# Performance work log

Measured on AMD Instinct MI355X. Metric: run time of the kernel, lower is better.

The kernel has to match this reference:

```python
import jax, jax.numpy as jnp
import numpy as np

B, T, H, DQK, DV = 2, 8192, 8, 128, 128
HID = H * DQK  # 1024
CHUNK = 64
EPS = 1e-5


def hedgehog(x, w, b):
    # torch Linear: y = x @ W.T + b, then softmax over cat([2y, -2y])
    y = x @ w.T + b
    return jax.nn.softmax(jnp.concatenate([2.0 * y, -2.0 * y], axis=-1), axis=-1)


def rmsnorm(x):
    return x * jax.lax.rsqrt(jnp.mean(x * x, axis=-1, keepdims=True) + EPS)


def chunk_linear_attn(q, k, v):
    # q, k: [B, T, H, Dk]; v: [B, T, H, Dv]  (head_first=False)
    scale = q.shape[-1] ** -0.5
    q = q * scale
    Bq, Tq, Hq, Dk = q.shape
    Dv = v.shape[-1]
    nc = Tq // CHUNK

    def to_chunks(t):
        # [B, T, H, D] -> [nc, B, H, C, D]
        return t.reshape(Bq, nc, CHUNK, Hq, -1).transpose(1, 0, 3, 2, 4)

    qc, kc, vc = to_chunks(q), to_chunks(k), to_chunks(v)
    mask = jnp.tril(jnp.ones((CHUNK, CHUNK), dtype=bool))

    def step(S, qkv):
        qi, ki, vi = qkv  # [B, H, C, D]
        attn = jnp.einsum('bhcd,bhed->bhce', qi, ki)      # intra-chunk scores
        attn = jnp.where(mask, attn, 0.0)                 # causal within chunk
        o = jnp.einsum('bhce,bhev->bhcv', attn, vi) \
            + jnp.einsum('bhcd,bhdv->bhcv', qi, S)        # inter-chunk via state
        S = S + jnp.einsum('bhcd,bhcv->bhdv', ki, vi)
        return S, o

    S0 = jnp.zeros((Bq, Hq, Dk, Dv), q.dtype)
    _, oc = jax.lax.scan(step, S0, (qc, kc, vc))          # oc: [nc, B, H, C, Dv]
    return oc.transpose(1, 0, 3, 2, 4).reshape(Bq, Tq, Hq, Dv)


def setup_inputs() -> dict:
    key = jax.random.key(0)
    ks = jax.random.split(key, 9)
    gain = 2.0 ** (-2.5)

    def xavier(k, shape):
        bound = gain * np.sqrt(6.0 / (shape[0] + shape[1]))
        return jax.random.uniform(k, shape, jnp.float32, -bound, bound)

    return {
        'x': jax.random.normal(ks[0], (B, T, HID), jnp.float32),
        'Wq': xavier(ks[1], (HID, HID)),
        'Wk': xavier(ks[2], (HID, HID)),
        'Wv': xavier(ks[3], (HID, HID)),
        'Wo': xavier(ks[4], (HID, HID)),
        # self.apply xavier-inits the hedgehog Linear layers too (no _is_hf_initialized flag)
        'fmq_w': xavier(ks[5], (DQK, DQK)),
        'fmq_b': jnp.zeros((DQK,), jnp.float32),
        'fmk_w': xavier(ks[6], (DQK, DQK)),
        'fmk_b': jnp.zeros((DQK,), jnp.float32),
    }


def reference(x, Wq, Wk, Wv, Wo, fmq_w, fmq_b, fmk_w, fmk_b):
    q = (x @ Wq.T).reshape(B, T, H, DQK)
    k = (x @ Wk.T).reshape(B, T, H, DQK)
    v = (x @ Wv.T).reshape(B, T, H, DV)
    q = hedgehog(q, fmq_w, fmq_b)   # [B, T, H, 2*DQK]
    k = hedgehog(k, fmk_w, fmk_b)   # [B, T, H, 2*DQK]
    o = chunk_linear_attn(q, k, v)  # [B, T, H, DV]
    o = rmsnorm(o.reshape(B, T, H * DV))
    return o @ Wo.T
```

## Files before the change

### kernel.cpp

```cpp
#include <hip/hip_runtime.h>
#include <stdint.h>

typedef unsigned short u16;
typedef __bf16 bf16x8 __attribute__((ext_vector_type(8)));
typedef float f32x4 __attribute__((ext_vector_type(4)));
typedef float f32x16 __attribute__((ext_vector_type(16)));

__device__ __forceinline__ u16 f2b(float f) {
  union { float f; unsigned u; } v; v.f = f;
  unsigned r = v.u + 0x7fffu + ((v.u >> 16) & 1u);
  return (u16)(r >> 16);
}
__device__ __forceinline__ float b2f(u16 b) {
  union { unsigned u; float f; } v; v.u = ((unsigned)b) << 16;
  return v.f;
}

__device__ __forceinline__ int swz64(int b) {
  return b ^ (((((b >> 6) & 3) ^ ((b >> 8) & 1))) << 4);
}

#define SB0() __builtin_amdgcn_sched_barrier(0)

__global__ __launch_bounds__(256) void cast_bf16(const float* __restrict__ in,
                                                 u16* __restrict__ out, int n4) {
  int i = blockIdx.x * 256 + threadIdx.x;
  if (i >= n4) return;
  float4 f = ((const float4*)in)[i];
  ushort4 r = make_ushort4(f2b(f.x), f2b(f.y), f2b(f.z), f2b(f.w));
  ((ushort4*)out)[i] = r;
}

__global__ __launch_bounds__(256) void fold_w(const float* __restrict__ W,
                                              const float* __restrict__ fmw,
                                              u16* __restrict__ out) {
  int hj = blockIdx.x;
  int h = hj >> 7, j = hj & 127;
  int i0 = threadIdx.x * 4;
  float a0 = 0.f, a1 = 0.f, a2 = 0.f, a3 = 0.f;
  const float* Wh = W + (size_t)(h * 128) * 1024 + i0;
  const float* fw = fmw + j * 128;
  for (int d = 0; d < 128; ++d) {
    float wv = fw[d];
    const float* wr = Wh + (size_t)d * 1024;
    a0 += wv * wr[0]; a1 += wv * wr[1]; a2 += wv * wr[2]; a3 += wv * wr[3];
  }
  ushort4 r = make_ushort4(f2b(a0), f2b(a1), f2b(a2), f2b(a3));
  ((ushort4*)(out + (size_t)hj * 1024))[threadIdx.x] = r;
}

__global__ __launch_bounds__(512, 2) void gemm256(const u16* __restrict__ A,
                                                  const u16* __restrict__ B,
                                                  u16* __restrict__ C,
                                                  int M, int N, int K, int LNT) {
  __shared__ u16 lds[65536];
  const int tid = threadIdx.x, w = tid >> 6, lane = tid & 63;
  int g = blockIdx.x;
  int wg = (g & 7) * ((int)gridDim.x >> 3) + (g >> 3);
  const int nt = wg & ((1 << LNT) - 1), mt = wg >> LNT;
  const int m0 = mt << 8, n0 = nt << 8;
  const int wm = w >> 2, wn = w & 3;
  const int fm = lane & 15, fkb = (lane >> 4) << 4;

  int so0 = w * 1024 + lane * 16;
  int so1 = so0 + 8192;
  const int p0s = swz64(so0), p1s = swz64(so1);
  const size_t ga0 = (size_t)(p0s >> 6) * K + ((p0s & 63) >> 1);
  const size_t ga1 = (size_t)(p1s >> 6) * K + ((p1s & 63) >> 1);
  so0 >>= 1; so1 >>= 1;
#define STAGE(g0, slot)                                                               \
  do {                                                                                \
    __builtin_amdgcn_global_load_lds(                                                 \
        (const __attribute__((address_space(1))) unsigned int*)((g0) + ga0),          \
        (__attribute__((address_space(3))) unsigned int*)((slot) + so0), 16, 0, 0);   \
    __builtin_amdgcn_global_load_lds(                                                 \
        (const __attribute__((address_space(1))) unsigned int*)((g0) + ga1),          \
        (__attribute__((address_space(3))) unsigned int*)((slot) + so1), 16, 0, 0);   \
  } while (0)

  int aoff[2][4], boff[4];
#pragma unroll
  for (int mh = 0; mh < 2; ++mh)
#pragma unroll
    for (int mi = 0; mi < 4; ++mi)
      aoff[mh][mi] = swz64((wm * 128 + mh * 64 + mi * 16 + fm) * 64 + fkb) >> 1;
#pragma unroll
  for (int ni = 0; ni < 4; ++ni)
    boff[ni] = swz64((wn * 64 + ni * 16 + fm) * 64 + fkb) >> 1;

  const u16* Ag = A + (size_t)m0 * K;
  const u16* Bg = B + (size_t)n0 * K;
  const int NT = K >> 6;
  f32x4 acc[8][4] = {};

  STAGE(Ag, lds);
  STAGE(Bg, lds + 32768);
  STAGE(Ag + 32, lds + 8192);
  STAGE(Bg + 32, lds + 32768 + 8192);
  STAGE(Ag + 64, lds + 16384);
  STAGE(Bg + 64, lds + 32768 + 16384);
  asm volatile("s_waitcnt vmcnt(4)" ::: "memory");
  __builtin_amdgcn_s_barrier();

  for (int t = 0; t < NT; ++t) {
    const int buf = t & 1, nb = buf ^ 1;
    const u16* As0 = lds + buf * 16384;
    const u16* As1 = As0 + 8192;
    const u16* Bs0 = lds + 32768 + buf * 16384;
    const u16* Bs1 = Bs0 + 8192;
    bf16x8 a[4], bfr[4];

#pragma unroll
    for (int mi = 0; mi < 4; ++mi) a[mi] = *(const bf16x8*)(As0 + aoff[0][mi]);
#pragma unroll
    for (int ni = 0; ni < 4; ++ni) bfr[ni] = *(const bf16x8*)(Bs0 + boff[ni]);
    if (t + 1 < NT) STAGE(Ag + (t + 1) * 64 + 32, lds + nb * 16384 + 8192);
    __builtin_amdgcn_s_barrier();
    asm volatile("s_waitcnt lgkmcnt(0)" ::: "memory");
    SB0();
    __builtin_amdgcn_s_setprio(1);
#pragma unroll
    for (int mi = 0; mi < 4; ++mi)
#pragma unroll
      for (int ni = 0; ni < 4; ++ni)
        acc[mi][ni] = __builtin_amdgcn_mfma_f32_16x16x32_bf16(a[mi], bfr[ni], acc[mi][ni], 0, 0, 0);
    __builtin_amdgcn_s_setprio(0);
    __builtin_amdgcn_s_barrier();

#pragma unroll
    for (int mi = 0; mi < 4; ++mi) a[mi] = *(const bf16x8*)(As0 + aoff[1][mi]);
    if (t + 1 < NT) STAGE(Bg + (t + 1) * 64 + 32, lds + 32768 + nb * 16384 + 8192);
    __builtin_amdgcn_s_barrier();
    asm volatile("s_waitcnt lgkmcnt(0)" ::: "memory");
    SB0();
    __builtin_amdgcn_s_setprio(1);
#pragma unroll
    for (int mi = 0; mi < 4; ++mi)
#pragma unroll
      for (int ni = 0; ni < 4; ++ni)
        acc[4 + mi][ni] =
            __builtin_amdgcn_mfma_f32_16x16x32_bf16(a[mi], bfr[ni], acc[4 + mi][ni], 0, 0, 0);
    __builtin_amdgcn_s_setprio(0);
    __builtin_amdgcn_s_barrier();

#pragma unroll
    for (int mi = 0; mi < 4; ++mi) a[mi] = *(const bf16x8*)(As1 + aoff[0][mi]);
#pragma unroll
    for (int ni = 0; ni < 4; ++ni) bfr[ni] = *(const bf16x8*)(Bs1 + boff[ni]);
    if (t + 2 < NT) STAGE(Ag + (t + 2) * 64, lds + buf * 16384);
    __builtin_amdgcn_s_barrier();
    asm volatile("s_waitcnt lgkmcnt(0)" ::: "memory");
    SB0();
    __builtin_amdgcn_s_setprio(1);
#pragma unroll
    for (int mi = 0; mi < 4; ++mi)
#pragma unroll
      for (int ni = 0; ni < 4; ++ni)
        acc[mi][ni] = __builtin_amdgcn_mfma_f32_16x16x32_bf16(a[mi], bfr[ni], acc[mi][ni], 0, 0, 0);
    __builtin_amdgcn_s_setprio(0);
    __builtin_amdgcn_s_barrier();

#pragma unroll
    for (int mi = 0; mi < 4; ++mi) a[mi] = *(const bf16x8*)(As1 + aoff[1][mi]);
    if (t + 2 < NT) STAGE(Bg + (t + 2) * 64, lds + 32768 + buf * 16384);
    __builtin_amdgcn_s_barrier();
    asm volatile("s_waitcnt lgkmcnt(0)" ::: "memory");
    SB0();
    __builtin_amdgcn_s_setprio(1);
#pragma unroll
    for (int mi = 0; mi < 4; ++mi)
#pragma unroll
      for (int ni = 0; ni < 4; ++ni)
        acc[4 + mi][ni] =
            __builtin_amdgcn_mfma_f32_16x16x32_bf16(a[mi], bfr[ni], acc[4 + mi][ni], 0, 0, 0);
    __builtin_amdgcn_s_setprio(0);
    if (t < NT - 2)
      asm volatile("s_waitcnt vmcnt(4)" ::: "memory");
    else
      asm volatile("s_waitcnt vmcnt(0)" ::: "memory");
    __builtin_amdgcn_s_barrier();
  }
#undef STAGE

  u16* Cs = lds;
  const int cr = (lane >> 4) << 2, cc = lane & 15;
#pragma unroll
  for (int am = 0; am < 8; ++am)
#pragma unroll
    for (int ni = 0; ni < 4; ++ni)
#pragma unroll
      for (int r = 0; r < 4; ++r)
        Cs[(wm * 128 + (am >> 2) * 64 + (am & 3) * 16 + cr + r) * 256 + wn * 64 + ni * 16 + cc] =
            f2b(acc[am][ni][r]);
  __syncthreads();
#pragma unroll
  for (int pass = 0; pass < 16; ++pass) {
    int row = pass * 16 + (tid >> 5);
    int colb = (tid & 31) << 4;
    *(uint4*)((char*)(C + (size_t)(m0 + row) * N + n0) + colb) =
        *(const uint4*)((const char*)(Cs + row * 256) + colb);
  }
}

template <int OUT_BF16>
__global__ __launch_bounds__(256) void gemm_bt(const u16* __restrict__ A,
                                               const u16* __restrict__ B,
                                               void* __restrict__ Cv,
                                               int M, int N, int K, int SWZ, int LNT) {
  __shared__ u16 smem[16384];
  u16* As = smem;
  u16* Bs = smem + 8192;
  const int tid = threadIdx.x;
  int g = blockIdx.y * gridDim.x + blockIdx.x;
  int xcd = g & 7, local = g >> 3;
  int mt, nt;
  if (SWZ == 0) {
    mt = xcd * ((int)gridDim.y >> 3) + (local >> LNT);
    nt = local & ((1 << LNT) - 1);
  } else {
    nt = xcd * ((int)gridDim.x >> 3) + (local >> 3);
    mt = local & 7;
  }
  const int m0 = mt * 128, n0 = nt * 128;
  const int wave = tid >> 6, lane = tid & 63;
  const int wm = (wave >> 1) << 6, wn = (wave & 1) << 6;
  f32x4 acc[4][4] = {};
  const int srow = tid >> 3;
  const int scol = (tid & 7) << 3;
  const u16* Ab = A + (size_t)(m0 + srow) * K + scol;
  const u16* Bb = B + (size_t)(n0 + srow) * K + scol;
  u16* Asp = As + srow * 64 + scol;
  u16* Bsp = Bs + srow * 64 + scol;
  const int fm = lane & 15;
  const int fk = (lane >> 4) << 3;
  for (int kt = 0; kt < K; kt += 64) {
#pragma unroll
    for (int i = 0; i < 4; ++i) {
      __builtin_amdgcn_global_load_lds(
          (__attribute__((address_space(1))) unsigned int*)(Ab + (size_t)i * 32 * K + kt),
          (__attribute__((address_space(3))) unsigned int*)(Asp + i * 32 * 64), 16, 0, 0);
      __builtin_amdgcn_global_load_lds(
          (__attribute__((address_space(1))) unsigned int*)(Bb + (size_t)i * 32 * K + kt),
          (__attribute__((address_space(3))) unsigned int*)(Bsp + i * 32 * 64), 16, 0, 0);
    }
    __syncthreads();
#pragma unroll
    for (int kb = 0; kb < 2; ++kb) {
      bf16x8 af[4], bfr[4];
#pragma unroll
      for (int i = 0; i < 4; ++i)
        af[i] = *(const bf16x8*)(As + (wm + i * 16 + fm) * 64 + kb * 32 + fk);
#pragma unroll
      for (int j = 0; j < 4; ++j)
        bfr[j] = *(const bf16x8*)(Bs + (wn + j * 16 + fm) * 64 + kb * 32 + fk);
#pragma unroll
      for (int i = 0; i < 4; ++i)
#pragma unroll
        for (int j = 0; j < 4; ++j)
          acc[i][j] = __builtin_amdgcn_mfma_f32_16x16x32_bf16(af[i], bfr[j], acc[i][j], 0, 0, 0);
    }
    __syncthreads();
  }
  const int cr = (lane >> 4) << 2;
  const int cc = lane & 15;
  if (OUT_BF16) {
    u16* Cs = smem;
#pragma unroll
    for (int i = 0; i < 4; ++i)
#pragma unroll
      for (int j = 0; j < 4; ++j)
#pragma unroll
        for (int r = 0; r < 4; ++r)
          Cs[(wm + i * 16 + cr + r) * 128 + wn + j * 16 + cc] = f2b(acc[i][j][r]);
    __syncthreads();
    u16* Cg = (u16*)Cv;
#pragma unroll
    for (int i = 0; i < 8; ++i) {
      int row = (i >> 1) * 32 + (tid >> 3);
      int col = ((i & 1) * 8 + (tid & 7)) * 8;
      *(uint4*)(Cg + (size_t)(m0 + row) * N + n0 + col) = *(const uint4*)(Cs + row * 128 + col);
    }
  } else {
    float* Csf = (float*)smem;
    float* Cg = (float*)Cv;
#pragma unroll
    for (int hh = 0; hh < 2; ++hh) {
      __syncthreads();
      if ((wm >> 6) == hh) {
#pragma unroll
        for (int i = 0; i < 4; ++i)
#pragma unroll
          for (int j = 0; j < 4; ++j)
#pragma unroll
            for (int r = 0; r < 4; ++r)
              Csf[(i * 16 + cr + r) * 128 + wn + j * 16 + cc] = acc[i][j][r];
      }
      __syncthreads();
#pragma unroll
      for (int i = 0; i < 8; ++i) {
        int row = (i >> 1) * 16 + (tid >> 4);
        int col = ((i & 1) * 16 + (tid & 15)) * 4;
        *(float4*)(Cg + (size_t)(m0 + hh * 64 + row) * N + n0 + col) =
            *(const float4*)(Csf + row * 128 + col);
      }
    }
  }
}

__global__ __launch_bounds__(256) void hedgehog_sm(const u16* __restrict__ y,
                                                   const float* __restrict__ bias,
                                                   u16* __restrict__ phi, float scale,
                                                   int colbase) {
  int wave = threadIdx.x >> 6, lane = threadIdx.x & 63;
  int rh = blockIdx.x * 4 + wave;
  const u16* yr = y + (size_t)(rh >> 3) * 2048 + colbase + (rh & 7) * 128;
  float a1 = 2.f * (b2f(yr[lane]) + bias[lane]);
  float a2 = 2.f * (b2f(yr[lane + 64]) + bias[lane + 64]);
  float mx = fmaxf(fabsf(a1), fabsf(a2));
#pragma unroll
  for (int off = 32; off; off >>= 1) mx = fmaxf(mx, __shfl_xor(mx, off, 64));
  float e1 = __expf(a1 - mx), e2 = __expf(a2 - mx);
  float n1 = __expf(-a1 - mx), n2 = __expf(-a2 - mx);
  float s = e1 + e2 + n1 + n2;
#pragma unroll
  for (int off = 32; off; off >>= 1) s += __shfl_xor(s, off, 64);
  float inv = scale / s;
  u16* pr = phi + (size_t)rh * 256;
  pr[lane] = f2b(e1 * inv);
  pr[lane + 64] = f2b(e2 * inv);
  pr[lane + 128] = f2b(n1 * inv);
  pr[lane + 192] = f2b(n2 * inv);
}

__global__ __launch_bounds__(256, 1) void attn_intra64(const u16* __restrict__ phi_q,
                                                       const u16* __restrict__ phi_k,
                                                       const u16* __restrict__ vt,
                                                       float* __restrict__ o,
                                                       u16* __restrict__ kv) {
  __shared__ u16 lds[18432];
  u16* At = lds;
  u16* Kt = lds;
  int g = blockIdx.x;
  int n = g & 127, h = g >> 7;
  int t0 = n * 64;
  const u16* qg = phi_q + ((size_t)t0 * 8 + h) * 256;
  const u16* kg = phi_k + ((size_t)t0 * 8 + h) * 256;
  const u16* vg = vt + (size_t)(h * 128) * 8192 + t0;
  int tid = threadIdx.x, lane = tid & 63, w = tid >> 6;
  const int fr = lane & 31, fg = (lane >> 5) << 3;
  const int rbase = (lane >> 5) << 2;
  const int mw = (w >> 1) << 5;
  const int nw = (w & 1) << 5;
  const int nv = (w & 1) << 6;

  f32x16 accS = {};
#pragma unroll
  for (int ks = 0; ks < 16; ++ks) {
    bf16x8 a = *(const bf16x8*)(qg + (size_t)(mw + fr) * 2048 + ks * 16 + fg);
    bf16x8 b = *(const bf16x8*)(kg + (size_t)(nw + fr) * 2048 + ks * 16 + fg);
    accS = __builtin_amdgcn_mfma_f32_32x32x16_bf16(a, b, accS, 0, 0, 0);
  }
  {
    int col = nw + (lane & 31);
#pragma unroll
    for (int r = 0; r < 16; ++r) {
      int row = mw + (r & 3) + ((r >> 2) << 3) + rbase;
      At[row * 136 + col] = f2b(col <= row ? accS[r] : 0.f);
    }
  }
  __syncthreads();
  f32x16 accO[2] = {};
#pragma unroll
  for (int ks = 0; ks < 4; ++ks) {
    bf16x8 a = *(const bf16x8*)(At + (mw + fr) * 136 + ks * 16 + fg);
#pragma unroll
    for (int nj = 0; nj < 2; ++nj) {
      bf16x8 b = *(const bf16x8*)(vg + (size_t)(nv + nj * 32 + fr) * 8192 + ks * 16 + fg);
      accO[nj] = __builtin_amdgcn_mfma_f32_32x32x16_bf16(a, b, accO[nj], 0, 0, 0);
    }
  }
  {
    float* og = o + ((size_t)t0 * 8 + h) * 128;
#pragma unroll
    for (int nj = 0; nj < 2; ++nj) {
      int vc = nv + nj * 32 + (lane & 31);
#pragma unroll
      for (int r = 0; r < 16; ++r) {
        int row = mw + (r & 3) + ((r >> 2) << 3) + rbase;
        og[(size_t)row * 1024 + vc] = accO[nj][r];
      }
    }
  }
  __syncthreads();

  {
    int r4 = (tid & 15) << 2;
    int d0 = (tid >> 4) << 4;
    u16 tmp[4][16];
#pragma unroll
    for (int r = 0; r < 4; ++r) {
      const u16* src = kg + (size_t)(r4 + r) * 2048 + d0;
      *(uint4*)(tmp[r]) = *(const uint4*)src;
      *(uint4*)(tmp[r] + 8) = *(const uint4*)(src + 8);
    }
#pragma unroll
    for (int jj = 0; jj < 16; ++jj) {
      ushort4 pk = make_ushort4(tmp[0][jj], tmp[1][jj], tmp[2][jj], tmp[3][jj]);
      *(ushort4*)(Kt + (d0 + jj) * 72 + r4) = pk;
    }
  }
  __syncthreads();
  const int nd = w << 6;
  f32x16 accKV[4][2] = {};
#pragma unroll
  for (int ks = 0; ks < 4; ++ks) {
    bf16x8 a[4], b[2];
#pragma unroll
    for (int mi = 0; mi < 4; ++mi)
      a[mi] = *(const bf16x8*)(vg + (size_t)(mi * 32 + fr) * 8192 + ks * 16 + fg);
#pragma unroll
    for (int nj = 0; nj < 2; ++nj)
      b[nj] = *(const bf16x8*)(Kt + (nd + nj * 32 + fr) * 72 + ks * 16 + fg);
#pragma unroll
    for (int mi = 0; mi < 4; ++mi)
#pragma unroll
      for (int nj = 0; nj < 2; ++nj)
        accKV[mi][nj] =
            __builtin_amdgcn_mfma_f32_32x32x16_bf16(a[mi], b[nj], accKV[mi][nj], 0, 0, 0);
  }
  {
    u16* kvg = kv + (size_t)g * 32768;
#pragma unroll
    for (int mi = 0; mi < 4; ++mi)
#pragma unroll
      for (int nj = 0; nj < 2; ++nj) {
        f32x16 acc = accKV[mi][nj];
        int d = nd + nj * 32 + (lane & 31);
#pragma unroll
        for (int r = 0; r < 16; ++r) {
          int vc = mi * 32 + (r & 3) + ((r >> 2) << 3) + rbase;
          kvg[(size_t)vc * 256 + d] = f2b(acc[r]);
        }
      }
  }
}

__global__ __launch_bounds__(256) void kv_scan64(u16* __restrict__ kv) {
  int idx = blockIdx.x * 256 + threadIdx.x;
  int h = idx >> 13;
  int e4 = idx & 8191;
  u16* p = kv + (size_t)h * 4194304 + (size_t)e4 * 4;
  float run[4] = {};
#pragma unroll 4
  for (int nn = 0; nn < 128; ++nn) {
    uint2 raw = *(const uint2*)p;
    u16* rv = (u16*)&raw;
    uint2 outw;
    u16* ov = (u16*)&outw;
#pragma unroll
    for (int i = 0; i < 4; ++i) {
      float v = b2f(rv[i]);
      ov[i] = f2b(run[i]);
      run[i] += v;
    }
    *(uint2*)p = outw;
    p += 32768;
  }
}

__global__ __launch_bounds__(256, 1) void attn_inter64(const u16* __restrict__ phi_q,
                                                       const u16* __restrict__ kv,
                                                       float* __restrict__ o) {
  int g = blockIdx.x;
  int n = g & 127, h = g >> 7;
  int t0 = n * 64;
  const u16* qg = phi_q + ((size_t)t0 * 8 + h) * 256;
  const u16* sg = kv + (size_t)g * 32768;
  int tid = threadIdx.x, lane = tid & 63, w = tid >> 6;
  const int fr = lane & 31, fg = (lane >> 5) << 3;
  const int rbase = (lane >> 5) << 2;
  const int mw = (w >> 1) << 5;
  const int nv = (w & 1) << 6;
  f32x16 acc[2] = {};
#pragma unroll
  for (int ks = 0; ks < 16; ++ks) {
    bf16x8 a = *(const bf16x8*)(qg + (size_t)(mw + fr) * 2048 + ks * 16 + fg);
#pragma unroll
    for (int nj = 0; nj < 2; ++nj) {
      bf16x8 b = *(const bf16x8*)(sg + (size_t)(nv + nj * 32 + fr) * 256 + ks * 16 + fg);
      acc[nj] = __builtin_amdgcn_mfma_f32_32x32x16_bf16(a, b, acc[nj], 0, 0, 0);
    }
  }
  float* og = o + ((size_t)t0 * 8 + h) * 128;
#pragma unroll
  for (int nj = 0; nj < 2; ++nj) {
    int vc = nv + nj * 32 + (lane & 31);
#pragma unroll
    for (int r = 0; r < 16; ++r) {
      int row = mw + (r & 3) + ((r >> 2) << 3) + rbase;
      og[(size_t)row * 1024 + vc] += acc[nj][r];
    }
  }
}

__global__ __launch_bounds__(256) void rmsnorm_k(const float* __restrict__ o,
                                                 u16* __restrict__ on) {
  __shared__ float red[4];
  int row = blockIdx.x;
  const float* orow = o + (size_t)row * 1024;
  int tid = threadIdx.x;
  float4 v = ((const float4*)orow)[tid];
  float ss = v.x * v.x + v.y * v.y + v.z * v.z + v.w * v.w;
#pragma unroll
  for (int off = 32; off; off >>= 1) ss += __shfl_xor(ss, off, 64);
  if ((tid & 63) == 0) red[tid >> 6] = ss;
  __syncthreads();
  float tot = red[0] + red[1] + red[2] + red[3];
  float rms = rsqrtf(tot * (1.f / 1024.f) + 1e-5f);
  ushort4 r = make_ushort4(f2b(v.x * rms), f2b(v.y * rms), f2b(v.z * rms), f2b(v.w * rms));
  ((ushort4*)(on + (size_t)row * 1024))[tid] = r;
}

extern "C" void kernel_launch(void* const* d_in, const int* in_sizes, int n_in,
                              void* d_out, int out_size, void* d_ws, size_t ws_size,
                              hipStream_t stream) {
  const float* x     = (const float*)d_in[0];
  const float* Wq    = (const float*)d_in[1];
  const float* Wk    = (const float*)d_in[2];
  const float* Wv    = (const float*)d_in[3];
  const float* Wo    = (const float*)d_in[4];
  const float* fmq_w = (const float*)d_in[5];
  const float* fmq_b = (const float*)d_in[6];
  const float* fmk_w = (const float*)d_in[7];
  const float* fmk_b = (const float*)d_in[8];

  char* ws = (char*)d_ws;
  u16*   kvb  = (u16*)(ws + 0);
  u16*   xb   = (u16*)(ws + 0);
  u16*   yb   = (u16*)(ws + 16777216);
  u16*   onb  = (u16*)(ws + 50331648);
  u16*   phiq = (u16*)(ws + 67108864);
  u16*   phik = (u16*)(ws + 100663296);
  u16*   vtb  = (u16*)(ws + 134217728);
  float* obuf = (float*)(ws + 150994944);
  u16*   wqkc = (u16*)(ws + 184549376);
  u16*   wvb  = (u16*)(ws + 188743680);
  u16*   wob  = (u16*)(ws + 190840832);

  cast_bf16<<<1024, 256, 0, stream>>>(Wv, wvb, 262144);
  cast_bf16<<<1024, 256, 0, stream>>>(Wo, wob, 262144);
  fold_w<<<1024, 256, 0, stream>>>(Wq, fmq_w, wqkc);
  fold_w<<<1024, 256, 0, stream>>>(Wk, fmk_w, wqkc + 1048576);

  for (int b = 0; b < 2; ++b) {
    const float* xsrc = x + (size_t)b * 8388608;
    float* osrc = (float*)d_out + (size_t)b * 8388608;
    cast_bf16<<<8192, 256, 0, stream>>>(xsrc, xb, 2097152);
    gemm256<<<256, 512, 0, stream>>>(xb, wqkc, yb, 8192, 2048, 1024, 3);
    hedgehog_sm<<<16384, 256, 0, stream>>>(yb, fmq_b, phiq, 0.0625f, 0);
    hedgehog_sm<<<16384, 256, 0, stream>>>(yb, fmk_b, phik, 1.0f, 1024);
    gemm_bt<1><<<dim3(64, 8), 256, 0, stream>>>(wvb, xb, vtb, 1024, 8192, 1024, 1, 0);
    attn_intra64<<<1024, 256, 0, stream>>>(phiq, phik, vtb, obuf, kvb);
    kv_scan64<<<256, 256, 0, stream>>>(kvb);
    attn_inter64<<<1024, 256, 0, stream>>>(phiq, kvb, obuf);
    rmsnorm_k<<<8192, 256, 0, stream>>>(obuf, onb);
    gemm_bt<0><<<dim3(8, 64), 256, 0, stream>>>(onb, wob, osrc, 8192, 1024, 1024, 0, 3);
  }
}
```

Measured before the change: 656.0 us.

## Reuse 256-tile GEMM for V and output projections; fuse intra and inter attention

The smaller 128-tile gemm_bt kernel is replaced by a templated gemm256 that can write fp32 output, and that kernel now handles both the V projection and the output projection. Attention is reorganised so one kernel computes only the per-chunk KV states. A fused kernel then computes the intra-chunk and inter-chunk outputs together and writes o once, instead of writing it and later doing a read-modify-write. The larger tiles give only 128 workgroups for 1024-wide N, so the GPU may be underfilled, and the intra scores are now computed after the scan.

```diff
diff --git a/kernel.cpp b/kernel.cpp
--- a/kernel.cpp
+++ b/kernel.cpp
@@ -49,9 +49,10 @@
   ((ushort4*)(out + (size_t)hj * 1024))[threadIdx.x] = r;
 }
 
+template <int OUT_BF16>
 __global__ __launch_bounds__(512, 2) void gemm256(const u16* __restrict__ A,
                                                   const u16* __restrict__ B,
-                                                  u16* __restrict__ C,
+                                                  void* __restrict__ Cv,
                                                   int M, int N, int K, int LNT) {
   __shared__ u16 lds[65536];
   const int tid = threadIdx.x, w = tid >> 6, lane = tid & 63;
@@ -182,126 +183,49 @@
   }
 #undef STAGE
 
-  u16* Cs = lds;
   const int cr = (lane >> 4) << 2, cc = lane & 15;
-#pragma unroll
-  for (int am = 0; am < 8; ++am)
-#pragma unroll
-    for (int ni = 0; ni < 4; ++ni)
-#pragma unroll
-      for (int r = 0; r < 4; ++r)
-        Cs[(wm * 128 + (am >> 2) * 64 + (am & 3) * 16 + cr + r) * 256 + wn * 64 + ni * 16 + cc] =
-            f2b(acc[am][ni][r]);
-  __syncthreads();
-#pragma unroll
-  for (int pass = 0; pass < 16; ++pass) {
-    int row = pass * 16 + (tid >> 5);
-    int colb = (tid & 31) << 4;
-    *(uint4*)((char*)(C + (size_t)(m0 + row) * N + n0) + colb) =
-        *(const uint4*)((const char*)(Cs + row * 256) + colb);
-  }
-}
-
-template <int OUT_BF16>
-__global__ __launch_bounds__(256) void gemm_bt(const u16* __restrict__ A,
-                                               const u16* __restrict__ B,
-                                               void* __restrict__ Cv,
-                                               int M, int N, int K, int SWZ, int LNT) {
-  __shared__ u16 smem[16384];
-  u16* As = smem;
-  u16* Bs = smem + 8192;
-  const int tid = threadIdx.x;
-  int g = blockIdx.y * gridDim.x + blockIdx.x;
-  int xcd = g & 7, local = g >> 3;
-  int mt, nt;
-  if (SWZ == 0) {
-    mt = xcd * ((int)gridDim.y >> 3) + (local >> LNT);
-    nt = local & ((1 << LNT) - 1);
+  if (OUT_BF16) {
+    u16* Cs = lds;
+    u16* Cg = (u16*)Cv;
+#pragma unroll
+    for (int am = 0; am < 8; ++am)
+#pragma unroll
+      for (int ni = 0; ni < 4; ++ni)
+#pragma unroll
+        for (int r = 0; r < 4; ++r)
+          Cs[(wm * 128 + (am >> 2) * 64 + (am & 3) * 16 + cr + r) * 256 + wn * 64 + ni * 16 + cc] =
+              f2b(acc[am][ni][r]);
+    __syncthreads();
+#pragma unroll
+    for (int pass = 0; pass < 16; ++pass) {
+      int row = pass * 16 + (tid >> 5);
+      int colb = (tid & 31) << 4;
+      *(uint4*)((char*)(Cg + (size_t)(m0 + row) * N + n0) + colb) =
+          *(const uint4*)((const char*)(Cs + row * 256) + colb);
+    }
   } else {
-    nt = xcd * ((int)gridDim.x >> 3) + (local >> 3);
-    mt = local & 7;
-  }
-  const int m0 = mt * 128, n0 = nt * 128;
-  const int wave = tid >> 6, lane = tid & 63;
-  const int wm = (wave >> 1) << 6, wn = (wave & 1) << 6;
-  f32x4 acc[4][4] = {};
-  const int srow = tid >> 3;
-  const int scol = (tid & 7) << 3;
-  const u16* Ab = A + (size_t)(m0 + srow) * K + scol;
-  const u16* Bb = B + (size_t)(n0 + srow) * K + scol;
-  u16* Asp = As + srow * 64 + scol;
-  u16* Bsp = Bs + srow * 64 + scol;
-  const int fm = lane & 15;
-  const int fk = (lane >> 4) << 3;
-  for (int kt = 0; kt < K; kt += 64) {
-#pragma unroll
-    for (int i = 0; i < 4; ++i) {
-      __builtin_amdgcn_global_load_lds(
-          (__attribute__((address_space(1))) unsigned int*)(Ab + (size_t)i * 32 * K + kt),
-          (__attribute__((address_space(3))) unsigned int*)(Asp + i * 32 * 64), 16, 0, 0);
-      __builtin_amdgcn_global_load_lds(
-          (__attribute__((address_space(1))) unsigned int*)(Bb + (size_t)i * 32 * K + kt),
-          (__attribute__((address_space(3))) unsigned int*)(Bsp + i * 32 * 64), 16, 0, 0);
-    }
-    __syncthreads();
-#pragma unroll
-    for (int kb = 0; kb < 2; ++kb) {
-      bf16x8 af[4], bfr[4];
-#pragma unroll
-      for (int i = 0; i < 4; ++i)
-        af[i] = *(const bf16x8*)(As + (wm + i * 16 + fm) * 64 + kb * 32 + fk);
-#pragma unroll
-      for (int j = 0; j < 4; ++j)
-        bfr[j] = *(const bf16x8*)(Bs + (wn + j * 16 + fm) * 64 + kb * 32 + fk);
-#pragma unroll
-      for (int i = 0; i < 4; ++i)
-#pragma unroll
-        for (int j = 0; j < 4; ++j)
-          acc[i][j] = __builtin_amdgcn_mfma_f32_16x16x32_bf16(af[i], bfr[j], acc[i][j], 0, 0, 0);
-    }
-    __syncthreads();
-  }
-  const int cr = (lane >> 4) << 2;
-  const int cc = lane & 15;
-  if (OUT_BF16) {
-    u16* Cs = smem;
-#pragma unroll
-    for (int i = 0; i < 4; ++i)
-#pragma unroll
-      for (int j = 0; j < 4; ++j)
-#pragma unroll
-        for (int r = 0; r < 4; ++r)
-          Cs[(wm + i * 16 + cr + r) * 128 + wn + j * 16 + cc] = f2b(acc[i][j][r]);
-    __syncthreads();
-    u16* Cg = (u16*)Cv;
-#pragma unroll
-    for (int i = 0; i < 8; ++i) {
-      int row = (i >> 1) * 32 + (tid >> 3);
-      int col = ((i & 1) * 8 + (tid & 7)) * 8;
-      *(uint4*)(Cg + (size_t)(m0 + row) * N + n0 + col) = *(const uint4*)(Cs + row * 128 + col);
-    }
-  } else {
-    float* Csf = (float*)smem;
+    float* Csf = (float*)lds;
     float* Cg = (float*)Cv;
 #pragma unroll
     for (int hh = 0; hh < 2; ++hh) {
       __syncthreads();
-      if ((wm >> 6) == hh) {
-#pragma unroll
-        for (int i = 0; i < 4; ++i)
-#pragma unroll
-          for (int j = 0; j < 4; ++j)
+      if (wm == hh) {
+#pragma unroll
+        for (int am = 0; am < 8; ++am)
+#pragma unroll
+          for (int ni = 0; ni < 4; ++ni)
 #pragma unroll
             for (int r = 0; r < 4; ++r)
-              Csf[(i * 16 + cr + r) * 128 + wn + j * 16 + cc] = acc[i][j][r];
+              Csf[((am >> 2) * 64 + (am & 3) * 16 + cr + r) * 256 + wn * 64 + ni * 16 + cc] =
+                  acc[am][ni][r];
       }
       __syncthreads();
 #pragma unroll
-      for (int i = 0; i < 8; ++i) {
-        int row = (i >> 1) * 16 + (tid >> 4);
-        int col = ((i & 1) * 16 + (tid & 15)) * 4;
-        *(float4*)(Cg + (size_t)(m0 + hh * 64 + row) * N + n0 + col) =
-            *(const float4*)(Csf + row * 128 + col);
+      for (int it = 0; it < 16; ++it) {
+        int row = it * 8 + (tid >> 6);
+        int colb = (tid & 63) << 2;
+        *(float4*)(Cg + (size_t)(m0 + hh * 128 + row) * N + n0 + colb) =
+            *(const float4*)(Csf + row * 256 + colb);
       }
     }
   }
@@ -332,66 +256,18 @@
   pr[lane + 192] = f2b(n2 * inv);
 }
 
-__global__ __launch_bounds__(256, 1) void attn_intra64(const u16* __restrict__ phi_q,
-                                                       const u16* __restrict__ phi_k,
-                                                       const u16* __restrict__ vt,
-                                                       float* __restrict__ o,
-                                                       u16* __restrict__ kv) {
-  __shared__ u16 lds[18432];
-  u16* At = lds;
-  u16* Kt = lds;
+__global__ __launch_bounds__(256, 1) void attn_kv64(const u16* __restrict__ phi_k,
+                                                    const u16* __restrict__ vt,
+                                                    u16* __restrict__ kv) {
+  __shared__ u16 Kt[18432];
   int g = blockIdx.x;
   int n = g & 127, h = g >> 7;
   int t0 = n * 64;
-  const u16* qg = phi_q + ((size_t)t0 * 8 + h) * 256;
   const u16* kg = phi_k + ((size_t)t0 * 8 + h) * 256;
   const u16* vg = vt + (size_t)(h * 128) * 8192 + t0;
   int tid = threadIdx.x, lane = tid & 63, w = tid >> 6;
   const int fr = lane & 31, fg = (lane >> 5) << 3;
   const int rbase = (lane >> 5) << 2;
-  const int mw = (w >> 1) << 5;
-  const int nw = (w & 1) << 5;
-  const int nv = (w & 1) << 6;
-
-  f32x16 accS = {};
-#pragma unroll
-  for (int ks = 0; ks < 16; ++ks) {
-    bf16x8 a = *(const bf16x8*)(qg + (size_t)(mw + fr) * 2048 + ks * 16 + fg);
-    bf16x8 b = *(const bf16x8*)(kg + (size_t)(nw + fr) * 2048 + ks * 16 + fg);
-    accS = __builtin_amdgcn_mfma_f32_32x32x16_bf16(a, b, accS, 0, 0, 0);
-  }
-  {
-    int col = nw + (lane & 31);
-#pragma unroll
-    for (int r = 0; r < 16; ++r) {
-      int row = mw + (r & 3) + ((r >> 2) << 3) + rbase;
-      At[row * 136 + col] = f2b(col <= row ? accS[r] : 0.f);
-    }
-  }
-  __syncthreads();
-  f32x16 accO[2] = {};
-#pragma unroll
-  for (int ks = 0; ks < 4; ++ks) {
-    bf16x8 a = *(const bf16x8*)(At + (mw + fr) * 136 + ks * 16 + fg);
-#pragma unroll
-    for (int nj = 0; nj < 2; ++nj) {
-      bf16x8 b = *(const bf16x8*)(vg + (size_t)(nv + nj * 32 + fr) * 8192 + ks * 16 + fg);
-      accO[nj] = __builtin_amdgcn_mfma_f32_32x32x16_bf16(a, b, accO[nj], 0, 0, 0);
-    }
-  }
-  {
-    float* og = o + ((size_t)t0 * 8 + h) * 128;
-#pragma unroll
-    for (int nj = 0; nj < 2; ++nj) {
-      int vc = nv + nj * 32 + (lane & 31);
-#pragma unroll
-      for (int r = 0; r < 16; ++r) {
-        int row = mw + (r & 3) + ((r >> 2) << 3) + rbase;
-        og[(size_t)row * 1024 + vc] = accO[nj][r];
-      }
-    }
-  }
-  __syncthreads();
 
   {
     int r4 = (tid & 15) << 2;
@@ -468,37 +344,71 @@
   }
 }
 
-__global__ __launch_bounds__(256, 1) void attn_inter64(const u16* __restrict__ phi_q,
+__global__ __launch_bounds__(256, 1) void attn_fused64(const u16* __restrict__ phi_q,
+                                                       const u16* __restrict__ phi_k,
+                                                       const u16* __restrict__ vt,
                                                        const u16* __restrict__ kv,
                                                        float* __restrict__ o) {
+  __shared__ u16 At[8704];
   int g = blockIdx.x;
   int n = g & 127, h = g >> 7;
   int t0 = n * 64;
   const u16* qg = phi_q + ((size_t)t0 * 8 + h) * 256;
+  const u16* kg = phi_k + ((size_t)t0 * 8 + h) * 256;
+  const u16* vg = vt + (size_t)(h * 128) * 8192 + t0;
   const u16* sg = kv + (size_t)g * 32768;
   int tid = threadIdx.x, lane = tid & 63, w = tid >> 6;
   const int fr = lane & 31, fg = (lane >> 5) << 3;
   const int rbase = (lane >> 5) << 2;
   const int mw = (w >> 1) << 5;
+  const int nw = (w & 1) << 5;
   const int nv = (w & 1) << 6;
-  f32x16 acc[2] = {};
+
+  f32x16 accS = {};
 #pragma unroll
   for (int ks = 0; ks < 16; ++ks) {
     bf16x8 a = *(const bf16x8*)(qg + (size_t)(mw + fr) * 2048 + ks * 16 + fg);
+    bf16x8 b = *(const bf16x8*)(kg + (size_t)(nw + fr) * 2048 + ks * 16 + fg);
+    accS = __builtin_amdgcn_mfma_f32_32x32x16_bf16(a, b, accS, 0, 0, 0);
+  }
+  {
+    int col = nw + (lane & 31);
+#pragma unroll
+    for (int r = 0; r < 16; ++r) {
+      int row = mw + (r & 3) + ((r >> 2) << 3) + rbase;
+      At[row * 136 + col] = f2b(col <= row ? accS[r] : 0.f);
+    }
+  }
+  __syncthreads();
+  f32x16 accO[2] = {};
+#pragma unroll
+  for (int ks = 0; ks < 4; ++ks) {
+    bf16x8 a = *(const bf16x8*)(At + (mw + fr) * 136 + ks * 16 + fg);
+#pragma unroll
+    for (int nj = 0; nj < 2; ++nj) {
+      bf16x8 b = *(const bf16x8*)(vg + (size_t)(nv + nj * 32 + fr) * 8192 + ks * 16 + fg);
+      accO[nj] = __builtin_amdgcn_mfma_f32_32x32x16_bf16(a, b, accO[nj], 0, 0, 0);
+    }
+  }
+#pragma unroll
+  for (int ks = 0; ks < 16; ++ks) {
+    bf16x8 a = *(const bf16x8*)(qg + (size_t)(mw + fr) * 2048 + ks * 16 + fg);
 #pragma unroll
     for (int nj = 0; nj < 2; ++nj) {
       bf16x8 b = *(const bf16x8*)(sg + (size_t)(nv + nj * 32 + fr) * 256 + ks * 16 + fg);
-      acc[nj] = __builtin_amdgcn_mfma_f32_32x32x16_bf16(a, b, acc[nj], 0, 0, 0);
-    }
-  }
-  float* og = o + ((size_t)t0 * 8 + h) * 128;
-#pragma unroll
-  for (int nj = 0; nj < 2; ++nj) {
-    int vc = nv + nj * 32 + (lane & 31);
-#pragma unroll
-    for (int r = 0; r < 16; ++r) {
-      int row = mw + (r & 3) + ((r >> 2) << 3) + rbase;
-      og[(size_t)row * 1024 + vc] += acc[nj][r];
+      accO[nj] = __builtin_amdgcn_mfma_f32_32x32x16_bf16(a, b, accO[nj], 0, 0, 0);
+    }
+  }
+  {
+    float* og = o + ((size_t)t0 * 8 + h) * 128;
+#pragma unroll
+    for (int nj = 0; nj < 2; ++nj) {
+      int vc = nv + nj * 32 + (lane & 31);
+#pragma unroll
+      for (int r = 0; r < 16; ++r) {
+        int row = mw + (r & 3) + ((r >> 2) << 3) + rbase;
+        og[(size_t)row * 1024 + vc] = accO[nj][r];
+      }
     }
   }
 }
@@ -556,14 +466,14 @@
     const float* xsrc = x + (size_t)b * 8388608;
     float* osrc = (float*)d_out + (size_t)b * 8388608;
     cast_bf16<<<8192, 256, 0, stream>>>(xsrc, xb, 2097152);
-    gemm256<<<256, 512, 0, stream>>>(xb, wqkc, yb, 8192, 2048, 1024, 3);
+    gemm256<1><<<256, 512, 0, stream>>>(xb, wqkc, yb, 8192, 2048, 1024, 3);
     hedgehog_sm<<<16384, 256, 0, stream>>>(yb, fmq_b, phiq, 0.0625f, 0);
     hedgehog_sm<<<16384, 256, 0, stream>>>(yb, fmk_b, phik, 1.0f, 1024);
-    gemm_bt<1><<<dim3(64, 8), 256, 0, stream>>>(wvb, xb, vtb, 1024, 8192, 1024, 1, 0);
-    attn_intra64<<<1024, 256, 0, stream>>>(phiq, phik, vtb, obuf, kvb);
+    gemm256<1><<<128, 512, 0, stream>>>(wvb, xb, vtb, 1024, 8192, 1024, 5);
+    attn_kv64<<<1024, 256, 0, stream>>>(phik, vtb, kvb);
     kv_scan64<<<256, 256, 0, stream>>>(kvb);
-    attn_inter64<<<1024, 256, 0, stream>>>(phiq, kvb, obuf);
+    attn_fused64<<<1024, 256, 0, stream>>>(phiq, phik, vtb, kvb, obuf);
     rmsnorm_k<<<8192, 256, 0, stream>>>(obuf, onb);
-    gemm_bt<0><<<dim3(8, 64), 256, 0, stream>>>(onb, wob, osrc, 8192, 1024, 1024, 0, 3);
-  }
-}
+    gemm256<0><<<128, 512, 0, stream>>>(onb, wob, osrc, 8192, 1024, 1024, 2);
+  }
+}
```

Result: slower. 702.5 us (+7.1%).

## Fuse intra-chunk attention with inter-chunk state product into one kernel

Applied to the files above, without the earlier changes.

Moves the intra-chunk QK^T and causal AV computation out of the KV-building kernel and into the inter-chunk kernel, which now computes Q·S and QK^T from Q fragments held in registers, then accumulates the masked AV into the same accumulators. This removes the fp32 write of the intra-chunk output followed by its read-modify-write in the inter kernel, and loads Q once instead of twice. The fused kernel uses more registers for the cached Q fragments, and the phi_k and V chunk reads now happen in both kernels.

```diff
diff --git a/kernel.cpp b/kernel.cpp
--- a/kernel.cpp
+++ b/kernel.cpp
@@ -332,66 +332,18 @@
   pr[lane + 192] = f2b(n2 * inv);
 }
 
-__global__ __launch_bounds__(256, 1) void attn_intra64(const u16* __restrict__ phi_q,
-                                                       const u16* __restrict__ phi_k,
-                                                       const u16* __restrict__ vt,
-                                                       float* __restrict__ o,
-                                                       u16* __restrict__ kv) {
-  __shared__ u16 lds[18432];
-  u16* At = lds;
-  u16* Kt = lds;
+__global__ __launch_bounds__(256, 1) void attn_kv64(const u16* __restrict__ phi_k,
+                                                    const u16* __restrict__ vt,
+                                                    u16* __restrict__ kv) {
+  __shared__ u16 Kt[18432];
   int g = blockIdx.x;
   int n = g & 127, h = g >> 7;
   int t0 = n * 64;
-  const u16* qg = phi_q + ((size_t)t0 * 8 + h) * 256;
   const u16* kg = phi_k + ((size_t)t0 * 8 + h) * 256;
   const u16* vg = vt + (size_t)(h * 128) * 8192 + t0;
   int tid = threadIdx.x, lane = tid & 63, w = tid >> 6;
   const int fr = lane & 31, fg = (lane >> 5) << 3;
   const int rbase = (lane >> 5) << 2;
-  const int mw = (w >> 1) << 5;
-  const int nw = (w & 1) << 5;
-  const int nv = (w & 1) << 6;
-
-  f32x16 accS = {};
-#pragma unroll
-  for (int ks = 0; ks < 16; ++ks) {
-    bf16x8 a = *(const bf16x8*)(qg + (size_t)(mw + fr) * 2048 + ks * 16 + fg);
-    bf16x8 b = *(const bf16x8*)(kg + (size_t)(nw + fr) * 2048 + ks * 16 + fg);
-    accS = __builtin_amdgcn_mfma_f32_32x32x16_bf16(a, b, accS, 0, 0, 0);
-  }
-  {
-    int col = nw + (lane & 31);
-#pragma unroll
-    for (int r = 0; r < 16; ++r) {
-      int row = mw + (r & 3) + ((r >> 2) << 3) + rbase;
-      At[row * 136 + col] = f2b(col <= row ? accS[r] : 0.f);
-    }
-  }
-  __syncthreads();
-  f32x16 accO[2] = {};
-#pragma unroll
-  for (int ks = 0; ks < 4; ++ks) {
-    bf16x8 a = *(const bf16x8*)(At + (mw + fr) * 136 + ks * 16 + fg);
-#pragma unroll
-    for (int nj = 0; nj < 2; ++nj) {
-      bf16x8 b = *(const bf16x8*)(vg + (size_t)(nv + nj * 32 + fr) * 8192 + ks * 16 + fg);
-      accO[nj] = __builtin_amdgcn_mfma_f32_32x32x16_bf16(a, b, accO[nj], 0, 0, 0);
-    }
-  }
-  {
-    float* og = o + ((size_t)t0 * 8 + h) * 128;
-#pragma unroll
-    for (int nj = 0; nj < 2; ++nj) {
-      int vc = nv + nj * 32 + (lane & 31);
-#pragma unroll
-      for (int r = 0; r < 16; ++r) {
-        int row = mw + (r & 3) + ((r >> 2) << 3) + rbase;
-        og[(size_t)row * 1024 + vc] = accO[nj][r];
-      }
-    }
-  }
-  __syncthreads();
 
   {
     int r4 = (tid & 15) << 2;
@@ -468,37 +420,77 @@
   }
 }
 
-__global__ __launch_bounds__(256, 1) void attn_inter64(const u16* __restrict__ phi_q,
+__global__ __launch_bounds__(256, 1) void attn_fused64(const u16* __restrict__ phi_q,
+                                                       const u16* __restrict__ phi_k,
+                                                       const u16* __restrict__ vt,
                                                        const u16* __restrict__ kv,
                                                        float* __restrict__ o) {
+  __shared__ u16 At[8704];
   int g = blockIdx.x;
   int n = g & 127, h = g >> 7;
   int t0 = n * 64;
   const u16* qg = phi_q + ((size_t)t0 * 8 + h) * 256;
+  const u16* kg = phi_k + ((size_t)t0 * 8 + h) * 256;
+  const u16* vg = vt + (size_t)(h * 128) * 8192 + t0;
   const u16* sg = kv + (size_t)g * 32768;
   int tid = threadIdx.x, lane = tid & 63, w = tid >> 6;
   const int fr = lane & 31, fg = (lane >> 5) << 3;
   const int rbase = (lane >> 5) << 2;
   const int mw = (w >> 1) << 5;
+  const int nw = (w & 1) << 5;
   const int nv = (w & 1) << 6;
-  f32x16 acc[2] = {};
-#pragma unroll
-  for (int ks = 0; ks < 16; ++ks) {
-    bf16x8 a = *(const bf16x8*)(qg + (size_t)(mw + fr) * 2048 + ks * 16 + fg);
-#pragma unroll
-    for (int nj = 0; nj < 2; ++nj) {
-      bf16x8 b = *(const bf16x8*)(sg + (size_t)(nv + nj * 32 + fr) * 256 + ks * 16 + fg);
-      acc[nj] = __builtin_amdgcn_mfma_f32_32x32x16_bf16(a, b, acc[nj], 0, 0, 0);
-    }
-  }
-  float* og = o + ((size_t)t0 * 8 + h) * 128;
-#pragma unroll
-  for (int nj = 0; nj < 2; ++nj) {
-    int vc = nv + nj * 32 + (lane & 31);
+
+  bf16x8 qf[16];
+  {
+    const u16* qrow = qg + (size_t)(mw + fr) * 2048 + fg;
+#pragma unroll
+    for (int ks = 0; ks < 16; ++ks) qf[ks] = *(const bf16x8*)(qrow + ks * 16);
+  }
+
+  f32x16 accS = {};
+  f32x16 accO[2] = {};
+  {
+    const u16* krow = kg + (size_t)(nw + fr) * 2048 + fg;
+    const u16* srow0 = sg + (size_t)(nv + fr) * 256 + fg;
+    const u16* srow1 = sg + (size_t)(nv + 32 + fr) * 256 + fg;
+#pragma unroll
+    for (int ks = 0; ks < 16; ++ks) {
+      bf16x8 kb = *(const bf16x8*)(krow + ks * 16);
+      bf16x8 sb0 = *(const bf16x8*)(srow0 + ks * 16);
+      bf16x8 sb1 = *(const bf16x8*)(srow1 + ks * 16);
+      accS = __builtin_amdgcn_mfma_f32_32x32x16_bf16(qf[ks], kb, accS, 0, 0, 0);
+      accO[0] = __builtin_amdgcn_mfma_f32_32x32x16_bf16(qf[ks], sb0, accO[0], 0, 0, 0);
+      accO[1] = __builtin_amdgcn_mfma_f32_32x32x16_bf16(qf[ks], sb1, accO[1], 0, 0, 0);
+    }
+  }
+  {
+    int col = nw + (lane & 31);
 #pragma unroll
     for (int r = 0; r < 16; ++r) {
       int row = mw + (r & 3) + ((r >> 2) << 3) + rbase;
-      og[(size_t)row * 1024 + vc] += acc[nj][r];
+      At[row * 136 + col] = f2b(col <= row ? accS[r] : 0.f);
+    }
+  }
+  __syncthreads();
+#pragma unroll
+  for (int ks = 0; ks < 4; ++ks) {
+    bf16x8 a = *(const bf16x8*)(At + (mw + fr) * 136 + ks * 16 + fg);
+#pragma unroll
+    for (int nj = 0; nj < 2; ++nj) {
+      bf16x8 b = *(const bf16x8*)(vg + (size_t)(nv + nj * 32 + fr) * 8192 + ks * 16 + fg);
+      accO[nj] = __builtin_amdgcn_mfma_f32_32x32x16_bf16(a, b, accO[nj], 0, 0, 0);
+    }
+  }
+  {
+    float* og = o + ((size_t)t0 * 8 + h) * 128;
+#pragma unroll
+    for (int nj = 0; nj < 2; ++nj) {
+      int vc = nv + nj * 32 + (lane & 31);
+#pragma unroll
+      for (int r = 0; r < 16; ++r) {
+        int row = mw + (r & 3) + ((r >> 2) << 3) + rbase;
+        og[(size_t)row * 1024 + vc] = accO[nj][r];
+      }
     }
   }
 }
@@ -560,9 +552,9 @@
     hedgehog_sm<<<16384, 256, 0, stream>>>(yb, fmq_b, phiq, 0.0625f, 0);
     hedgehog_sm<<<16384, 256, 0, stream>>>(yb, fmk_b, phik, 1.0f, 1024);
     gemm_bt<1><<<dim3(64, 8), 256, 0, stream>>>(wvb, xb, vtb, 1024, 8192, 1024, 1, 0);
-    attn_intra64<<<1024, 256, 0, stream>>>(phiq, phik, vtb, obuf, kvb);
+    attn_kv64<<<1024, 256, 0, stream>>>(phik, vtb, kvb);
     kv_scan64<<<256, 256, 0, stream>>>(kvb);
-    attn_inter64<<<1024, 256, 0, stream>>>(phiq, kvb, obuf);
+    attn_fused64<<<1024, 256, 0, stream>>>(phiq, phik, vtb, kvb, obuf);
     rmsnorm_k<<<8192, 256, 0, stream>>>(obuf, onb);
     gemm_bt<0><<<dim3(8, 64), 256, 0, stream>>>(onb, wob, osrc, 8192, 1024, 1024, 0, 3);
   }
```

Result: no change. 643.4 us (-1.9%).
